# Performance work log

Measured on AMD Instinct MI355X. Metric: run time of the kernel, lower is better.

## Reference

```python
import jax, jax.numpy as jnp
import numpy as np

EPS = 1e-5
NEG_SLOPE = 0.01
GROUPS = 8


def leaky(x):
    return jnp.where(x >= 0, x, NEG_SLOPE * x)


def group_norm(x, gamma, beta):
    # torchsparse GroupNorm on a single-batch sparse tensor: normalize over
    # all points and the channels within each group. x: [N, C]
    N, C = x.shape
    xg = x.reshape(N, GROUPS, C // GROUPS)
    mean = xg.mean(axis=(0, 2), keepdims=True)
    var = xg.var(axis=(0, 2), keepdims=True)
    xn = ((xg - mean) * jax.lax.rsqrt(var + EPS)).reshape(N, C)
    return xn * gamma + beta


def spconv(feats, W, in_map, out_map, n_out):
    # Rulebook gather -> per-offset GEMM -> scatter-add.
    # feats: [N_in, Cin], W: [K, Cin, Cout], in_map/out_map: [K, M]
    Cout = W.shape[-1]
    g = feats[in_map]                               # [K, M, Cin] gather
    c = jnp.einsum('kmc,kcd->kmd', g, W)            # [K, M, Cout]
    out = jnp.zeros((n_out, Cout), feats.dtype)
    return out.at[out_map.reshape(-1)].add(c.reshape(-1, Cout))


def residual_block(h, Wa, ga, ba, Wb, gb, bb, m_in, m_out, n_out):
    y = group_norm(spconv(h, Wa, m_in, m_out, n_out), ga, ba)
    y = group_norm(spconv(y, Wb, m_in, m_out, n_out), gb, bb)
    return leaky(y + h)  # identity downsample (inc==outc, stride==1)


def setup_inputs() -> dict:
    key = jax.random.key(0)
    ks = jax.random.split(key, 12)
    N_in, N_out, C = 600000, 150000, 64
    M1, M2 = 75000, 60000
    sc = 0.05
    inp = {
        'x': jax.random.normal(ks[0], (N_in, C), jnp.float32),
        'W1': jax.random.normal(ks[1], (8, C, C), jnp.float32) * sc,
        'g1': jnp.ones((C,), jnp.float32), 'b1': jnp.zeros((C,), jnp.float32),
        'Wa1': jax.random.normal(ks[2], (27, C, C), jnp.float32) * sc,
        'ga1': jnp.ones((C,), jnp.float32), 'ba1': jnp.zeros((C,), jnp.float32),
        'Wb1': jax.random.normal(ks[3], (27, C, C), jnp.float32) * sc,
        'gb1': jnp.ones((C,), jnp.float32), 'bb1': jnp.zeros((C,), jnp.float32),
        'Wa2': jax.random.normal(ks[4], (27, C, C), jnp.float32) * sc,
        'ga2': jnp.ones((C,), jnp.float32), 'ba2': jnp.zeros((C,), jnp.float32),
        'Wb2': jax.random.normal(ks[5], (27, C, C), jnp.float32) * sc,
        'gb2': jnp.ones((C,), jnp.float32), 'bb2': jnp.zeros((C,), jnp.float32),
        'm1_in': jax.random.randint(ks[6], (8, M1), 0, N_in, jnp.int32),
        'm1_out': jax.random.randint(ks[7], (8, M1), 0, N_out, jnp.int32),
        'm2_in': jax.random.randint(ks[8], (27, M2), 0, N_out, jnp.int32),
        'm2_out': jax.random.randint(ks[9], (27, M2), 0, N_out, jnp.int32),
        'n_out': N_out,
    }
    return inp


def reference(x, W1, g1, b1, Wa1, ga1, ba1, Wb1, gb1, bb1,
              Wa2, ga2, ba2, Wb2, gb2, bb2,
              m1_in, m1_out, m2_in, m2_out, n_out):
    # BasicConvolutionBlock: Conv3d(ks=2, stride=2) -> GroupNorm(8) -> LeakyReLU
    h = leaky(group_norm(spconv(x, W1, m1_in, m1_out, n_out), g1, b1))
    # ResidualBlock x2: (Conv3d ks=3 -> GN -> Conv3d ks=3 -> GN) + identity, LeakyReLU
    h = residual_block(h, Wa1, ga1, ba1, Wb1, gb1, bb1, m2_in, m2_out, n_out)
    h = residual_block(h, Wa2, ga2, ba2, Wb2, gb2, bb2, m2_in, m2_out, n_out)
    return h
```

## Files before the change

### kernel.cpp

```cpp
#include <hip/hip_runtime.h>

#define NEG_SLOPE 0.01f
#define GN_EPS 1e-5f

typedef __attribute__((ext_vector_type(8))) __bf16 bf16x8;
typedef __attribute__((ext_vector_type(4))) __bf16 bf16x4;
typedef __attribute__((ext_vector_type(4))) float f32x4;
typedef __attribute__((ext_vector_type(2))) unsigned uintx2;

__device__ __forceinline__ float bf_lo(unsigned v) { return __uint_as_float(v << 16); }
__device__ __forceinline__ float bf_hi(unsigned v) { return __uint_as_float(v & 0xffff0000u); }

__global__ __launch_bounds__(256) void hist_kernel(
    const int* __restrict__ om, int* __restrict__ cnt, int E)
{
    const int stride = gridDim.x * blockDim.x;
    for (int e = blockIdx.x * blockDim.x + threadIdx.x; e < E; e += stride)
        atomicAdd(&cnt[om[e]], 1);
}

__global__ __launch_bounds__(256) void scan1_kernel(
    const int* __restrict__ cnt, int* __restrict__ part, int N)
{
    __shared__ int ls[256];
    int b = blockIdx.x, t = threadIdx.x;
    int i0 = b * 1024 + t * 4, s = 0;
#pragma unroll
    for (int u = 0; u < 4; ++u) if (i0 + u < N) s += cnt[i0 + u];
    ls[t] = s; __syncthreads();
    for (int off = 128; off > 0; off >>= 1) {
        if (t < off) ls[t] += ls[t + off];
        __syncthreads();
    }
    if (t == 0) part[b] = ls[0];
}

__global__ void scan2_kernel(int* __restrict__ part, int nb)
{
    if (blockIdx.x == 0 && threadIdx.x == 0) {
        int run = 0;
        for (int i = 0; i < nb; ++i) { int v = part[i]; part[i] = run; run += v; }
    }
}

__global__ __launch_bounds__(256) void scan3_kernel(
    const int* __restrict__ cnt, const int* __restrict__ part,
    int* __restrict__ base, int N)
{
    __shared__ int ls[256];
    int b = blockIdx.x, t = threadIdx.x;
    int i0 = b * 1024 + t * 4;
    int v0 = 0, v1 = 0, v2 = 0, v3 = 0;
    if (i0 + 0 < N) v0 = cnt[i0 + 0];
    if (i0 + 1 < N) v1 = cnt[i0 + 1];
    if (i0 + 2 < N) v2 = cnt[i0 + 2];
    if (i0 + 3 < N) v3 = cnt[i0 + 3];
    int s = v0 + v1 + v2 + v3;
    ls[t] = s; __syncthreads();
    for (int off = 1; off < 256; off <<= 1) {
        int x = (t >= off) ? ls[t - off] : 0;
        __syncthreads();
        ls[t] += x;
        __syncthreads();
    }
    int run = part[b] + ls[t] - s;
    if (i0 + 0 < N) { base[i0 + 0] = run; run += v0; if (i0 + 0 == N - 1) base[N] = run; }
    if (i0 + 1 < N) { base[i0 + 1] = run; run += v1; if (i0 + 1 == N - 1) base[N] = run; }
    if (i0 + 2 < N) { base[i0 + 2] = run; run += v2; if (i0 + 2 == N - 1) base[N] = run; }
    if (i0 + 3 < N) { base[i0 + 3] = run; run += v3; if (i0 + 3 == N - 1) base[N] = run; }
}

__global__ __launch_bounds__(256) void scatter_kernel(
    const int* __restrict__ om, const int* __restrict__ base,
    int* __restrict__ cur, int* __restrict__ inv, int E)
{
    const int stride = gridDim.x * blockDim.x;
    for (int e = blockIdx.x * blockDim.x + threadIdx.x; e < E; e += stride) {
        int o = om[e];
        int p = base[o] + atomicAdd(&cur[o], 1);
        inv[e] = p;
    }
}

template<int F32IN>
__global__ __launch_bounds__(256) void conv_mfma_kernel(
    const void* __restrict__ feats, const float* __restrict__ W,
    const int* __restrict__ in_map, const int* __restrict__ inv,
    __bf16* __restrict__ C, int M, int BPK)
{
    const int lane = threadIdx.x & 63;
    const int wv   = threadIdx.x >> 6;
    const int k    = blockIdx.x / BPK;
    const int blk  = blockIdx.x % BPK;
    const int l15  = lane & 15;
    const int lg   = lane >> 4;

    const float* Wk = W + (size_t)k * 4096;
    bf16x8 b[4][2];
#pragma unroll
    for (int nt = 0; nt < 4; ++nt)
#pragma unroll
        for (int h = 0; h < 2; ++h)
#pragma unroll
            for (int j = 0; j < 8; ++j)
                b[nt][h][j] = (__bf16)Wk[(h * 32 + lg * 8 + j) * 64 + nt * 16 + l15];

    const int* imk   = in_map + (size_t)k * M;
    const int ntiles = (M + 15) >> 4;
    const int wpk    = BPK * 4;

    for (int t = blk * 4 + wv; t < ntiles; t += wpk) {
        int m  = t * 16 + l15;
        int mc = m < M ? m : M - 1;
        int ii = imk[mc];
        bf16x8 a0, a1;
        if (F32IN) {
            const float4* rp = (const float4*)((const float*)feats + (size_t)ii * 64 + lg * 8);
            float4 u0 = rp[0], u1 = rp[1];
            float4 u2 = rp[8], u3 = rp[9];
            a0[0] = (__bf16)u0.x; a0[1] = (__bf16)u0.y; a0[2] = (__bf16)u0.z; a0[3] = (__bf16)u0.w;
            a0[4] = (__bf16)u1.x; a0[5] = (__bf16)u1.y; a0[6] = (__bf16)u1.z; a0[7] = (__bf16)u1.w;
            a1[0] = (__bf16)u2.x; a1[1] = (__bf16)u2.y; a1[2] = (__bf16)u2.z; a1[3] = (__bf16)u2.w;
            a1[4] = (__bf16)u3.x; a1[5] = (__bf16)u3.y; a1[6] = (__bf16)u3.z; a1[7] = (__bf16)u3.w;
        } else {
            const bf16x8* rp = (const bf16x8*)((const __bf16*)feats + (size_t)ii * 64 + lg * 8);
            a0 = rp[0];
            a1 = rp[4];
        }
        f32x4 c0 = {0.f,0.f,0.f,0.f}, c1 = c0, c2 = c0, c3 = c0;
        c0 = __builtin_amdgcn_mfma_f32_16x16x32_bf16(a0, b[0][0], c0, 0, 0, 0);
        c1 = __builtin_amdgcn_mfma_f32_16x16x32_bf16(a0, b[1][0], c1, 0, 0, 0);
        c2 = __builtin_amdgcn_mfma_f32_16x16x32_bf16(a0, b[2][0], c2, 0, 0, 0);
        c3 = __builtin_amdgcn_mfma_f32_16x16x32_bf16(a0, b[3][0], c3, 0, 0, 0);
        c0 = __builtin_amdgcn_mfma_f32_16x16x32_bf16(a1, b[0][1], c0, 0, 0, 0);
        c1 = __builtin_amdgcn_mfma_f32_16x16x32_bf16(a1, b[1][1], c1, 0, 0, 0);
        c2 = __builtin_amdgcn_mfma_f32_16x16x32_bf16(a1, b[2][1], c2, 0, 0, 0);
        c3 = __builtin_amdgcn_mfma_f32_16x16x32_bf16(a1, b[3][1], c3, 0, 0, 0);

        const int e_base = k * M + t * 16;
        f32x4 cc[4] = {c0, c1, c2, c3};
#pragma unroll
        for (int r = 0; r < 4; ++r) {
            int row = lg * 4 + r;
            if (t * 16 + row < M) {
                int p = inv[e_base + row];
                __bf16* cr = C + (size_t)p * 64 + l15;
#pragma unroll
                for (int nt = 0; nt < 4; ++nt) {
                    __bf16 v = (__bf16)cc[nt][r];
                    __builtin_nontemporal_store(v, cr + nt * 16);
                }
            }
        }
    }
}

__global__ __launch_bounds__(256) void reduce_kernel(
    const unsigned* __restrict__ C2, const int* __restrict__ base,
    float* __restrict__ out, float* __restrict__ stats, int N)
{
    const int lane = threadIdx.x & 63;
    const int wv   = threadIdx.x >> 6;
    const int rq   = lane >> 4;
    const int cq   = lane & 15;
    float rs = 0.f, rqsum = 0.f;

    const int ostride = gridDim.x * 4;
    for (int o = blockIdx.x * 4 + wv; o < N; o += ostride) {
        const int s = base[o], t = base[o + 1];
        float a0 = 0.f, a1 = 0.f, a2 = 0.f, a3 = 0.f;
        for (int i = s + rq; i < t; i += 4) {
            uintx2 v = __builtin_nontemporal_load(
                (const uintx2*)(C2 + (size_t)i * 32 + cq * 2));
            a0 += bf_lo(v.x); a1 += bf_hi(v.x);
            a2 += bf_lo(v.y); a3 += bf_hi(v.y);
        }
        a0 += __shfl_xor(a0, 16); a1 += __shfl_xor(a1, 16);
        a2 += __shfl_xor(a2, 16); a3 += __shfl_xor(a3, 16);
        a0 += __shfl_xor(a0, 32); a1 += __shfl_xor(a1, 32);
        a2 += __shfl_xor(a2, 32); a3 += __shfl_xor(a3, 32);
        if (rq == 0) {
            float4 r = {a0, a1, a2, a3};
            *(float4*)(out + (size_t)o * 64 + cq * 4) = r;
            rs    += (a0 + a1) + (a2 + a3);
            rqsum += (a0 * a0 + a1 * a1) + (a2 * a2 + a3 * a3);
        }
    }
    rs += __shfl_xor(rs, 1); rqsum += __shfl_xor(rqsum, 1);
    __shared__ float ls[4][16];
    if (rq == 0 && (cq & 1) == 0) {
        ls[wv][cq >> 1] = rs;
        ls[wv][8 + (cq >> 1)] = rqsum;
    }
    __syncthreads();
    if (threadIdx.x < 16) {
        float t = (ls[0][threadIdx.x] + ls[1][threadIdx.x]) +
                  (ls[2][threadIdx.x] + ls[3][threadIdx.x]);
        unsafeAtomicAdd(stats + threadIdx.x, t);
    }
}

__global__ __launch_bounds__(256) void conv_kernel(
    const float* __restrict__ feats, const float* __restrict__ W,
    const int* __restrict__ in_map, const int* __restrict__ out_map,
    float* __restrict__ out, int M, int BPK)
{
    const int lane = threadIdx.x & 63;
    const int wv   = threadIdx.x >> 6;
    const int k    = blockIdx.x / BPK;
    const int blk  = blockIdx.x % BPK;
    const float* Wk = W + (size_t)k * 4096;
    float w[64];
#pragma unroll
    for (int c = 0; c < 64; ++c) w[c] = Wk[c * 64 + lane];
    __shared__ float fbuf[4][64];
    const int* im = in_map + (size_t)k * M;
    const int* om = out_map + (size_t)k * M;
    const int stride = BPK * 4;
    for (int m = blk * 4 + wv; m < M; m += stride) {
        int ii = im[m];
        int oi = om[m];
        float f = feats[(size_t)ii * 64 + lane];
        fbuf[wv][lane] = f;
        const float* fb = fbuf[wv];
        float a0 = 0.f, a1 = 0.f, a2 = 0.f, a3 = 0.f;
#pragma unroll
        for (int c = 0; c < 64; c += 4) {
            float4 f4 = *(const float4*)(fb + c);
            a0 = fmaf(f4.x, w[c + 0], a0);
            a1 = fmaf(f4.y, w[c + 1], a1);
            a2 = fmaf(f4.z, w[c + 2], a2);
            a3 = fmaf(f4.w, w[c + 3], a3);
        }
        unsafeAtomicAdd(out + (size_t)oi * 64 + lane, (a0 + a1) + (a2 + a3));
    }
}

__global__ __launch_bounds__(256) void gn_stats_kernel(
    const float4* __restrict__ x, float* __restrict__ stats, long total4)
{
    const int lane = threadIdx.x & 63;
    float s = 0.f, q = 0.f;
    const long stride = (long)gridDim.x * blockDim.x;
    for (long i = (long)blockIdx.x * blockDim.x + threadIdx.x; i < total4; i += stride) {
        float4 v = x[i];
        s += (v.x + v.y) + (v.z + v.w);
        q += (v.x * v.x + v.y * v.y) + (v.z * v.z + v.w * v.w);
    }
    s += __shfl_xor(s, 1);  q += __shfl_xor(q, 1);
    s += __shfl_xor(s, 16); q += __shfl_xor(q, 16);
    s += __shfl_xor(s, 32); q += __shfl_xor(q, 32);
    __shared__ float ls[4][16];
    const int wv = threadIdx.x >> 6;
    const int g = (lane >> 1) & 7;
    if (lane < 16 && (lane & 1) == 0) { ls[wv][g] = s; ls[wv][8 + g] = q; }
    __syncthreads();
    if (threadIdx.x < 16) {
        float t = (ls[0][threadIdx.x] + ls[1][threadIdx.x]) +
                  (ls[2][threadIdx.x] + ls[3][threadIdx.x]);
        unsafeAtomicAdd(stats + threadIdx.x, t);
    }
}

__global__ __launch_bounds__(256) void gn_apply_kernel(
    const float4* __restrict__ x, const float* __restrict__ stats,
    const float* __restrict__ gamma, const float* __restrict__ beta,
    const float4* resid, float4* out_f, bf16x4* out_bf,
    long total4, float invc, int do_leaky)
{
    __shared__ float sc[64], sh[64];
    if (threadIdx.x < 64) {
        int c = threadIdx.x, g = c >> 3;
        float mean = stats[g] * invc;
        float var  = fmaf(-mean, mean, stats[8 + g] * invc);
        float s    = rsqrtf(var + GN_EPS) * gamma[c];
        sc[c] = s;
        sh[c] = fmaf(-mean, s, beta[c]);
    }
    __syncthreads();
    const long stride = (long)gridDim.x * blockDim.x;
    for (long i = (long)blockIdx.x * blockDim.x + threadIdx.x; i < total4; i += stride) {
        float4 v = x[i];
        int c0 = ((int)(i & 15)) << 2;
        float4 r;
        r.x = fmaf(v.x, sc[c0 + 0], sh[c0 + 0]);
        r.y = fmaf(v.y, sc[c0 + 1], sh[c0 + 1]);
        r.z = fmaf(v.z, sc[c0 + 2], sh[c0 + 2]);
        r.w = fmaf(v.w, sc[c0 + 3], sh[c0 + 3]);
        if (resid) {
            float4 h4 = resid[i];
            r.x += h4.x; r.y += h4.y; r.z += h4.z; r.w += h4.w;
        }
        if (do_leaky) {
            r.x = r.x >= 0.f ? r.x : NEG_SLOPE * r.x;
            r.y = r.y >= 0.f ? r.y : NEG_SLOPE * r.y;
            r.z = r.z >= 0.f ? r.z : NEG_SLOPE * r.z;
            r.w = r.w >= 0.f ? r.w : NEG_SLOPE * r.w;
        }
        if (out_f) out_f[i] = r;
        if (out_bf) {
            bf16x4 o;
            o.x = (__bf16)r.x; o.y = (__bf16)r.y; o.z = (__bf16)r.z; o.w = (__bf16)r.w;
            out_bf[i] = o;
        }
    }
}

extern "C" void kernel_launch(void* const* d_in, const int* in_sizes, int n_in,
                              void* d_out, int out_size, void* d_ws, size_t ws_size,
                              hipStream_t stream) {
    const float* x   = (const float*)d_in[0];
    const float* W1  = (const float*)d_in[1];
    const float* g1  = (const float*)d_in[2];
    const float* b1  = (const float*)d_in[3];
    const float* Wa1 = (const float*)d_in[4];
    const float* ga1 = (const float*)d_in[5];
    const float* ba1 = (const float*)d_in[6];
    const float* Wb1 = (const float*)d_in[7];
    const float* gb1 = (const float*)d_in[8];
    const float* bb1 = (const float*)d_in[9];
    const float* Wa2 = (const float*)d_in[10];
    const float* ga2 = (const float*)d_in[11];
    const float* ba2 = (const float*)d_in[12];
    const float* Wb2 = (const float*)d_in[13];
    const float* gb2 = (const float*)d_in[14];
    const float* bb2 = (const float*)d_in[15];
    const int* m1_in  = (const int*)d_in[16];
    const int* m1_out = (const int*)d_in[17];
    const int* m2_in  = (const int*)d_in[18];
    const int* m2_out = (const int*)d_in[19];

    const int N   = out_size / 64;
    const int M1  = in_sizes[16] / 8;
    const int M2  = in_sizes[18] / 27;
    const int E1  = 8 * M1;
    const int E2  = 27 * M2;
    const int Emax = E1 > E2 ? E1 : E2;

    float* h = (float*)d_out;
    const long  total4 = (long)N * 16;
    const float invc   = 1.f / ((float)N * 8.f);

    char* wp = (char*)d_ws;
    size_t off = 0;
    auto alloc = [&](size_t bytes) {
        void* p = wp + off;
        off = (off + bytes + 255) & ~(size_t)255;
        return p;
    };
    float*  acc   = (float*)alloc((size_t)N * 64 * 4);
    __bf16* hbf   = (__bf16*)alloc((size_t)N * 64 * 2);
    __bf16* ybf   = (__bf16*)alloc((size_t)N * 64 * 2);
    __bf16* Cbuf  = (__bf16*)alloc((size_t)Emax * 64 * 2);
    int*    base1 = (int*)alloc((size_t)(N + 1) * 4);
    int*    base2 = (int*)alloc((size_t)(N + 1) * 4);
    int*    cnt   = (int*)alloc((size_t)N * 4);
    int*    part  = (int*)alloc(4096);
    int*    inv1  = (int*)alloc((size_t)E1 * 4);
    int*    inv2  = (int*)alloc((size_t)E2 * 4);
    float*  stats = (float*)alloc(5 * 16 * 4);
    const size_t need = off;

    if (ws_size < need) {
        float* y  = (float*)Cbuf;
        float* st = stats;
        const size_t nbytes = (size_t)N * 64 * 4;
        auto convL = [&](const float* feats, const float* W, const int* im,
                         const int* om, int K, int M, int BPK) {
            hipMemsetAsync(acc, 0, nbytes, stream);
            conv_kernel<<<dim3(K * BPK), 256, 0, stream>>>(feats, W, im, om, acc, M, BPK);
        };
        auto gnL = [&](const float* gamma, const float* beta, const float* resid,
                       float* outp, int leaky) {
            hipMemsetAsync(st, 0, 16 * sizeof(float), stream);
            gn_stats_kernel<<<1024, 256, 0, stream>>>((const float4*)acc, st, total4);
            gn_apply_kernel<<<1024, 256, 0, stream>>>((const float4*)acc, st, gamma, beta,
                                                      (const float4*)resid, (float4*)outp,
                                                      nullptr, total4, invc, leaky);
        };
        convL(x, W1, m1_in, m1_out, 8, M1, 320); gnL(g1, b1, nullptr, h, 1);
        convL(h, Wa1, m2_in, m2_out, 27, M2, 96); gnL(ga1, ba1, nullptr, y, 0);
        convL(y, Wb1, m2_in, m2_out, 27, M2, 96); gnL(gb1, bb1, h, h, 1);
        convL(h, Wa2, m2_in, m2_out, 27, M2, 96); gnL(ga2, ba2, nullptr, y, 0);
        convL(y, Wb2, m2_in, m2_out, 27, M2, 96); gnL(gb2, bb2, h, h, 1);
        return;
    }

    hipMemsetAsync(stats, 0, 5 * 16 * sizeof(float), stream);

    const int nb = (N + 1023) / 1024;
    auto buildCSR = [&](const int* om, int E, int* base, int* inv) {
        hipMemsetAsync(cnt, 0, (size_t)N * 4, stream);
        hist_kernel<<<2048, 256, 0, stream>>>(om, cnt, E);
        scan1_kernel<<<nb, 256, 0, stream>>>(cnt, part, N);
        scan2_kernel<<<1, 64, 0, stream>>>(part, nb);
        scan3_kernel<<<nb, 256, 0, stream>>>(cnt, part, base, N);
        hipMemsetAsync(cnt, 0, (size_t)N * 4, stream);
        scatter_kernel<<<2048, 256, 0, stream>>>(om, base, cnt, inv, E);
    };
    buildCSR(m1_out, E1, base1, inv1);
    buildCSR(m2_out, E2, base2, inv2);

    float* st0  = stats;
    float* stA1 = stats + 16;
    float* stB1 = stats + 32;
    float* stA2 = stats + 48;
    float* stB2 = stats + 64;

    auto conv = [&](const void* feats, int f32in, const float* W, const int* im,
                    int K, int M, int BPK, const int* base, const int* inv,
                    float* statOut) {
        dim3 grid(K * BPK);
        if (f32in)
            conv_mfma_kernel<1><<<grid, 256, 0, stream>>>(feats, W, im, inv, Cbuf, M, BPK);
        else
            conv_mfma_kernel<0><<<grid, 256, 0, stream>>>(feats, W, im, inv, Cbuf, M, BPK);
        reduce_kernel<<<2048, 256, 0, stream>>>((const unsigned*)Cbuf, base,
                                                acc, statOut, N);
    };
    auto gn = [&](const float* st, const float* gamma, const float* beta,
                  const float* resid, float* outf, __bf16* outbf, int leaky) {
        gn_apply_kernel<<<1024, 256, 0, stream>>>((const float4*)acc, st, gamma, beta,
                                                  (const float4*)resid, (float4*)outf,
                                                  (bf16x4*)outbf, total4, invc, leaky);
    };

    conv(x, 1, W1, m1_in, 8, M1, 256, base1, inv1, st0);
    gn(st0, g1, b1, nullptr, h, hbf, 1);
    conv(hbf, 0, Wa1, m2_in, 27, M2, 96, base2, inv2, stA1);
    gn(stA1, ga1, ba1, nullptr, nullptr, ybf, 0);
    conv(ybf, 0, Wb1, m2_in, 27, M2, 96, base2, inv2, stB1);
    gn(stB1, gb1, bb1, h, h, hbf, 1);
    conv(hbf, 0, Wa2, m2_in, 27, M2, 96, base2, inv2, stA2);
    gn(stA2, ga2, ba2, nullptr, nullptr, ybf, 0);
    conv(ybf, 0, Wb2, m2_in, 27, M2, 96, base2, inv2, stB2);
    gn(stB2, gb2, bb2, h, h, nullptr, 1);
}
```

Baseline: 1.078 ms.

## Bin rulebook entries by output tile and offset to localize conv scatter writes

Adds a second counting-sort pass that groups rulebook entries by (output-row tile of 1024, kernel offset). The MFMA conv kernel then runs one block per bin, so each block's scattered writes into the CSR-ordered C buffer fall in a narrow address range, which should improve write locality. The reduce output accumulator also moves from fp32 to bf16, roughly halving that traffic at some precision cost in the pre-GroupNorm values. The price is extra preprocessing kernels and index arrays, plus load imbalance from many small bins.

After: 1.635 ms. 1.52x slower.

```diff
diff --git a/kernel.cpp b/kernel.cpp
--- a/kernel.cpp
+++ b/kernel.cpp
@@ -2,6 +2,7 @@
 
 #define NEG_SLOPE 0.01f
 #define GN_EPS 1e-5f
+#define SSH 10
 
 typedef __attribute__((ext_vector_type(8))) __bf16 bf16x8;
 typedef __attribute__((ext_vector_type(4))) __bf16 bf16x4;
@@ -82,18 +83,47 @@
     }
 }
 
+__global__ __launch_bounds__(256) void histB_kernel(
+    const int* __restrict__ om, int* __restrict__ cnt, int M, int TK, int BPK)
+{
+    int k = blockIdx.x / BPK, blk = blockIdx.x % BPK;
+    const int* omk = om + (size_t)k * M;
+    for (int m = blk * 256 + threadIdx.x; m < M; m += BPK * 256)
+        atomicAdd(&cnt[(omk[m] >> SSH) * TK + k], 1);
+}
+
+__global__ __launch_bounds__(256) void scatterB_kernel(
+    const int* __restrict__ om, const int* __restrict__ im,
+    const int* __restrict__ inv, const int* __restrict__ baseB,
+    int* __restrict__ curB, int* __restrict__ im2, int* __restrict__ pv2,
+    int M, int TK, int BPK)
+{
+    int k = blockIdx.x / BPK, blk = blockIdx.x % BPK;
+    const int* omk  = om  + (size_t)k * M;
+    const int* imk  = im  + (size_t)k * M;
+    const int* invk = inv + (size_t)k * M;
+    for (int m = blk * 256 + threadIdx.x; m < M; m += BPK * 256) {
+        int key = (omk[m] >> SSH) * TK + k;
+        int pos = baseB[key] + atomicAdd(&curB[key], 1);
+        im2[pos] = imk[m];
+        pv2[pos] = invk[m];
+    }
+}
+
 template<int F32IN>
-__global__ __launch_bounds__(256) void conv_mfma_kernel(
+__global__ __launch_bounds__(256) void conv_bin_kernel(
     const void* __restrict__ feats, const float* __restrict__ W,
-    const int* __restrict__ in_map, const int* __restrict__ inv,
-    __bf16* __restrict__ C, int M, int BPK)
-{
+    const int* __restrict__ im2, const int* __restrict__ pv2,
+    const int* __restrict__ baseB, __bf16* __restrict__ C, int TK)
+{
+    const int bin  = blockIdx.x;
+    const int k    = bin % TK;
     const int lane = threadIdx.x & 63;
     const int wv   = threadIdx.x >> 6;
-    const int k    = blockIdx.x / BPK;
-    const int blk  = blockIdx.x % BPK;
     const int l15  = lane & 15;
     const int lg   = lane >> 4;
+    const int s = baseB[bin], e = baseB[bin + 1];
+    if (s >= e) return;
 
     const float* Wk = W + (size_t)k * 4096;
     bf16x8 b[4][2];
@@ -105,14 +135,11 @@
             for (int j = 0; j < 8; ++j)
                 b[nt][h][j] = (__bf16)Wk[(h * 32 + lg * 8 + j) * 64 + nt * 16 + l15];
 
-    const int* imk   = in_map + (size_t)k * M;
-    const int ntiles = (M + 15) >> 4;
-    const int wpk    = BPK * 4;
-
-    for (int t = blk * 4 + wv; t < ntiles; t += wpk) {
-        int m  = t * 16 + l15;
-        int mc = m < M ? m : M - 1;
-        int ii = imk[mc];
+    for (int cb = s + wv * 16; cb < e; cb += 64) {
+        const int idx = cb + l15;
+        const int idc = idx < e ? idx : e - 1;
+        const int ii  = im2[idc];
+        const int pv  = pv2[idc];
         bf16x8 a0, a1;
         if (F32IN) {
             const float4* rp = (const float4*)((const float*)feats + (size_t)ii * 64 + lg * 8);
@@ -137,13 +164,12 @@
         c2 = __builtin_amdgcn_mfma_f32_16x16x32_bf16(a1, b[2][1], c2, 0, 0, 0);
         c3 = __builtin_amdgcn_mfma_f32_16x16x32_bf16(a1, b[3][1], c3, 0, 0, 0);
 
-        const int e_base = k * M + t * 16;
         f32x4 cc[4] = {c0, c1, c2, c3};
 #pragma unroll
         for (int r = 0; r < 4; ++r) {
-            int row = lg * 4 + r;
-            if (t * 16 + row < M) {
-                int p = inv[e_base + row];
+            const int row = lg * 4 + r;
+            if (cb + row < e) {
+                int p = __shfl(pv, row);
                 __bf16* cr = C + (size_t)p * 64 + l15;
 #pragma unroll
                 for (int nt = 0; nt < 4; ++nt) {
@@ -157,7 +183,7 @@
 
 __global__ __launch_bounds__(256) void reduce_kernel(
     const unsigned* __restrict__ C2, const int* __restrict__ base,
-    float* __restrict__ out, float* __restrict__ stats, int N)
+    __bf16* __restrict__ out, float* __restrict__ stats, int N)
 {
     const int lane = threadIdx.x & 63;
     const int wv   = threadIdx.x >> 6;
@@ -180,8 +206,9 @@
         a0 += __shfl_xor(a0, 32); a1 += __shfl_xor(a1, 32);
         a2 += __shfl_xor(a2, 32); a3 += __shfl_xor(a3, 32);
         if (rq == 0) {
-            float4 r = {a0, a1, a2, a3};
-            *(float4*)(out + (size_t)o * 64 + cq * 4) = r;
+            bf16x4 r;
+            r.x = (__bf16)a0; r.y = (__bf16)a1; r.z = (__bf16)a2; r.w = (__bf16)a3;
+            *(bf16x4*)(out + (size_t)o * 64 + cq * 4) = r;
             rs    += (a0 + a1) + (a2 + a3);
             rqsum += (a0 * a0 + a1 * a1) + (a2 * a2 + a3 * a3);
         }
@@ -197,6 +224,57 @@
         float t = (ls[0][threadIdx.x] + ls[1][threadIdx.x]) +
                   (ls[2][threadIdx.x] + ls[3][threadIdx.x]);
         unsafeAtomicAdd(stats + threadIdx.x, t);
+    }
+}
+
+template<int BFIN>
+__global__ __launch_bounds__(256) void gn_apply_kernel(
+    const void* __restrict__ xin, const float* __restrict__ stats,
+    const float* __restrict__ gamma, const float* __restrict__ beta,
+    const float4* resid, float4* out_f, bf16x4* out_bf,
+    long total4, float invc, int do_leaky)
+{
+    __shared__ float sc[64], sh[64];
+    if (threadIdx.x < 64) {
+        int c = threadIdx.x, g = c >> 3;
+        float mean = stats[g] * invc;
+        float var  = fmaf(-mean, mean, stats[8 + g] * invc);
+        float s    = rsqrtf(var + GN_EPS) * gamma[c];
+        sc[c] = s;
+        sh[c] = fmaf(-mean, s, beta[c]);
+    }
+    __syncthreads();
+    const long stride = (long)gridDim.x * blockDim.x;
+    for (long i = (long)blockIdx.x * blockDim.x + threadIdx.x; i < total4; i += stride) {
+        float4 v;
+        if (BFIN) {
+            bf16x4 u = ((const bf16x4*)xin)[i];
+            v.x = (float)u.x; v.y = (float)u.y; v.z = (float)u.z; v.w = (float)u.w;
+        } else {
+            v = ((const float4*)xin)[i];
+        }
+        int c0 = ((int)(i & 15)) << 2;
+        float4 r;
+        r.x = fmaf(v.x, sc[c0 + 0], sh[c0 + 0]);
+        r.y = fmaf(v.y, sc[c0 + 1], sh[c0 + 1]);
+        r.z = fmaf(v.z, sc[c0 + 2], sh[c0 + 2]);
+        r.w = fmaf(v.w, sc[c0 + 3], sh[c0 + 3]);
+        if (resid) {
+            float4 h4 = resid[i];
+            r.x += h4.x; r.y += h4.y; r.z += h4.z; r.w += h4.w;
+        }
+        if (do_leaky) {
+            r.x = r.x >= 0.f ? r.x : NEG_SLOPE * r.x;
+            r.y = r.y >= 0.f ? r.y : NEG_SLOPE * r.y;
+            r.z = r.z >= 0.f ? r.z : NEG_SLOPE * r.z;
+            r.w = r.w >= 0.f ? r.w : NEG_SLOPE * r.w;
+        }
+        if (out_f) out_f[i] = r;
+        if (out_bf) {
+            bf16x4 o;
+            o.x = (__bf16)r.x; o.y = (__bf16)r.y; o.z = (__bf16)r.z; o.w = (__bf16)r.w;
+            out_bf[i] = o;
+        }
     }
 }
 
@@ -259,50 +337,6 @@
         float t = (ls[0][threadIdx.x] + ls[1][threadIdx.x]) +
                   (ls[2][threadIdx.x] + ls[3][threadIdx.x]);
         unsafeAtomicAdd(stats + threadIdx.x, t);
-    }
-}
-
-__global__ __launch_bounds__(256) void gn_apply_kernel(
-    const float4* __restrict__ x, const float* __restrict__ stats,
-    const float* __restrict__ gamma, const float* __restrict__ beta,
-    const float4* resid, float4* out_f, bf16x4* out_bf,
-    long total4, float invc, int do_leaky)
-{
-    __shared__ float sc[64], sh[64];
-    if (threadIdx.x < 64) {
-        int c = threadIdx.x, g = c >> 3;
-        float mean = stats[g] * invc;
-        float var  = fmaf(-mean, mean, stats[8 + g] * invc);
-        float s    = rsqrtf(var + GN_EPS) * gamma[c];
-        sc[c] = s;
-        sh[c] = fmaf(-mean, s, beta[c]);
-    }
-    __syncthreads();
-    const long stride = (long)gridDim.x * blockDim.x;
-    for (long i = (long)blockIdx.x * blockDim.x + threadIdx.x; i < total4; i += stride) {
-        float4 v = x[i];
-        int c0 = ((int)(i & 15)) << 2;
-        float4 r;
-        r.x = fmaf(v.x, sc[c0 + 0], sh[c0 + 0]);
-        r.y = fmaf(v.y, sc[c0 + 1], sh[c0 + 1]);
-        r.z = fmaf(v.z, sc[c0 + 2], sh[c0 + 2]);
-        r.w = fmaf(v.w, sc[c0 + 3], sh[c0 + 3]);
-        if (resid) {
-            float4 h4 = resid[i];
-            r.x += h4.x; r.y += h4.y; r.z += h4.z; r.w += h4.w;
-        }
-        if (do_leaky) {
-            r.x = r.x >= 0.f ? r.x : NEG_SLOPE * r.x;
-            r.y = r.y >= 0.f ? r.y : NEG_SLOPE * r.y;
-            r.z = r.z >= 0.f ? r.z : NEG_SLOPE * r.z;
-            r.w = r.w >= 0.f ? r.w : NEG_SLOPE * r.w;
-        }
-        if (out_f) out_f[i] = r;
-        if (out_bf) {
-            bf16x4 o;
-            o.x = (__bf16)r.x; o.y = (__bf16)r.y; o.z = (__bf16)r.z; o.w = (__bf16)r.w;
-            out_bf[i] = o;
-        }
     }
 }
 
@@ -336,6 +370,9 @@
     const int E1  = 8 * M1;
     const int E2  = 27 * M2;
     const int Emax = E1 > E2 ? E1 : E2;
+    const int tilesS = (N + (1 << SSH) - 1) >> SSH;
+    const int NB1 = tilesS * 8;
+    const int NB2 = tilesS * 27;
 
     float* h = (float*)d_out;
     const long  total4 = (long)N * 16;
@@ -348,58 +385,80 @@
         off = (off + bytes + 255) & ~(size_t)255;
         return p;
     };
-    float*  acc   = (float*)alloc((size_t)N * 64 * 4);
-    __bf16* hbf   = (__bf16*)alloc((size_t)N * 64 * 2);
-    __bf16* ybf   = (__bf16*)alloc((size_t)N * 64 * 2);
-    __bf16* Cbuf  = (__bf16*)alloc((size_t)Emax * 64 * 2);
-    int*    base1 = (int*)alloc((size_t)(N + 1) * 4);
-    int*    base2 = (int*)alloc((size_t)(N + 1) * 4);
-    int*    cnt   = (int*)alloc((size_t)N * 4);
-    int*    part  = (int*)alloc(4096);
-    int*    inv1  = (int*)alloc((size_t)E1 * 4);
-    int*    inv2  = (int*)alloc((size_t)E2 * 4);
-    float*  stats = (float*)alloc(5 * 16 * 4);
+    __bf16* accbf  = (__bf16*)alloc((size_t)N * 64 * 2);
+    __bf16* hbf    = (__bf16*)alloc((size_t)N * 64 * 2);
+    __bf16* ybf    = (__bf16*)alloc((size_t)N * 64 * 2);
+    __bf16* Cbuf   = (__bf16*)alloc((size_t)Emax * 64 * 2);
+    int*    base1  = (int*)alloc((size_t)(N + 1) * 4);
+    int*    base2  = (int*)alloc((size_t)(N + 1) * 4);
+    int*    cnt    = (int*)alloc((size_t)N * 4);
+    int*    part   = (int*)alloc(4096);
+    int*    inv1   = (int*)alloc((size_t)E1 * 4);
+    int*    inv2   = (int*)alloc((size_t)E2 * 4);
+    int*    baseB1 = (int*)alloc((size_t)(NB1 + 1) * 4);
+    int*    baseB2 = (int*)alloc((size_t)(NB2 + 1) * 4);
+    int*    im2_1  = (int*)alloc((size_t)E1 * 4);
+    int*    pv2_1  = (int*)alloc((size_t)E1 * 4);
+    int*    im2_2  = (int*)alloc((size_t)E2 * 4);
+    int*    pv2_2  = (int*)alloc((size_t)E2 * 4);
+    float*  stats  = (float*)alloc(5 * 16 * 4);
     const size_t need = off;
 
     if (ws_size < need) {
-        float* y  = (float*)Cbuf;
-        float* st = stats;
+        float* accF = (float*)d_ws;
+        float* yF   = accF + (size_t)N * 64;
+        float* stF  = yF + (size_t)N * 64;
         const size_t nbytes = (size_t)N * 64 * 4;
         auto convL = [&](const float* feats, const float* W, const int* im,
                          const int* om, int K, int M, int BPK) {
-            hipMemsetAsync(acc, 0, nbytes, stream);
-            conv_kernel<<<dim3(K * BPK), 256, 0, stream>>>(feats, W, im, om, acc, M, BPK);
+            hipMemsetAsync(accF, 0, nbytes, stream);
+            conv_kernel<<<dim3(K * BPK), 256, 0, stream>>>(feats, W, im, om, accF, M, BPK);
         };
         auto gnL = [&](const float* gamma, const float* beta, const float* resid,
                        float* outp, int leaky) {
-            hipMemsetAsync(st, 0, 16 * sizeof(float), stream);
-            gn_stats_kernel<<<1024, 256, 0, stream>>>((const float4*)acc, st, total4);
-            gn_apply_kernel<<<1024, 256, 0, stream>>>((const float4*)acc, st, gamma, beta,
-                                                      (const float4*)resid, (float4*)outp,
-                                                      nullptr, total4, invc, leaky);
+            hipMemsetAsync(stF, 0, 16 * sizeof(float), stream);
+            gn_stats_kernel<<<1024, 256, 0, stream>>>((const float4*)accF, stF, total4);
+            gn_apply_kernel<0><<<1024, 256, 0, stream>>>(accF, stF, gamma, beta,
+                                                         (const float4*)resid, (float4*)outp,
+                                                         nullptr, total4, invc, leaky);
         };
         convL(x, W1, m1_in, m1_out, 8, M1, 320); gnL(g1, b1, nullptr, h, 1);
-        convL(h, Wa1, m2_in, m2_out, 27, M2, 96); gnL(ga1, ba1, nullptr, y, 0);
-        convL(y, Wb1, m2_in, m2_out, 27, M2, 96); gnL(gb1, bb1, h, h, 1);
-        convL(h, Wa2, m2_in, m2_out, 27, M2, 96); gnL(ga2, ba2, nullptr, y, 0);
-        convL(y, Wb2, m2_in, m2_out, 27, M2, 96); gnL(gb2, bb2, h, h, 1);
+        convL(h, Wa1, m2_in, m2_out, 27, M2, 96); gnL(ga1, ba1, nullptr, yF, 0);
+        convL(yF, Wb1, m2_in, m2_out, 27, M2, 96); gnL(gb1, bb1, h, h, 1);
+        convL(h, Wa2, m2_in, m2_out, 27, M2, 96); gnL(ga2, ba2, nullptr, yF, 0);
+        convL(yF, Wb2, m2_in, m2_out, 27, M2, 96); gnL(gb2, bb2, h, h, 1);
         return;
     }
 
     hipMemsetAsync(stats, 0, 5 * 16 * sizeof(float), stream);
 
-    const int nb = (N + 1023) / 1024;
+    const int nbN = (N + 1023) / 1024;
     auto buildCSR = [&](const int* om, int E, int* base, int* inv) {
         hipMemsetAsync(cnt, 0, (size_t)N * 4, stream);
         hist_kernel<<<2048, 256, 0, stream>>>(om, cnt, E);
-        scan1_kernel<<<nb, 256, 0, stream>>>(cnt, part, N);
-        scan2_kernel<<<1, 64, 0, stream>>>(part, nb);
-        scan3_kernel<<<nb, 256, 0, stream>>>(cnt, part, base, N);
+        scan1_kernel<<<nbN, 256, 0, stream>>>(cnt, part, N);
+        scan2_kernel<<<1, 64, 0, stream>>>(part, nbN);
+        scan3_kernel<<<nbN, 256, 0, stream>>>(cnt, part, base, N);
         hipMemsetAsync(cnt, 0, (size_t)N * 4, stream);
         scatter_kernel<<<2048, 256, 0, stream>>>(om, base, cnt, inv, E);
     };
+    auto buildBins = [&](const int* om, const int* im, const int* inv, int M,
+                         int TK, int NB, int* baseB, int* im2, int* pv2) {
+        const int BPK = 48;
+        const int nbB = (NB + 1023) / 1024;
+        hipMemsetAsync(cnt, 0, (size_t)NB * 4, stream);
+        histB_kernel<<<dim3(TK * BPK), 256, 0, stream>>>(om, cnt, M, TK, BPK);
+        scan1_kernel<<<nbB, 256, 0, stream>>>(cnt, part, NB);
+        scan2_kernel<<<1, 64, 0, stream>>>(part, nbB);
+        scan3_kernel<<<nbB, 256, 0, stream>>>(cnt, part, baseB, NB);
+        hipMemsetAsync(cnt, 0, (size_t)NB * 4, stream);
+        scatterB_kernel<<<dim3(TK * BPK), 256, 0, stream>>>(om, im, inv, baseB, cnt,
+                                                            im2, pv2, M, TK, BPK);
+    };
     buildCSR(m1_out, E1, base1, inv1);
     buildCSR(m2_out, E2, base2, inv2);
+    buildBins(m1_out, m1_in, inv1, M1, 8, NB1, baseB1, im2_1, pv2_1);
+    buildBins(m2_out, m2_in, inv2, M2, 27, NB2, baseB2, im2_2, pv2_2);
 
     float* st0  = stats;
     float* stA1 = stats + 16;
@@ -407,32 +466,31 @@
     float* stA2 = stats + 48;
     float* stB2 = stats + 64;
 
-    auto conv = [&](const void* feats, int f32in, const float* W, const int* im,
-                    int K, int M, int BPK, const int* base, const int* inv,
-                    float* statOut) {
-        dim3 grid(K * BPK);
+    auto conv = [&](const void* feats, int f32in, const float* W, int TK, int NB,
+                    const int* im2, const int* pv2, const int* baseB,
+                    const int* base, float* statOut) {
         if (f32in)
-            conv_mfma_kernel<1><<<grid, 256, 0, stream>>>(feats, W, im, inv, Cbuf, M, BPK);
+            conv_bin_kernel<1><<<NB, 256, 0, stream>>>(feats, W, im2, pv2, baseB, Cbuf, TK);
         else
-            conv_mfma_kernel<0><<<grid, 256, 0, stream>>>(feats, W, im, inv, Cbuf, M, BPK);
+            conv_bin_kernel<0><<<NB, 256, 0, stream>>>(feats, W, im2, pv2, baseB, Cbuf, TK);
         reduce_kernel<<<2048, 256, 0, stream>>>((const unsigned*)Cbuf, base,
-                                                acc, statOut, N);
+                                                accbf, statOut, N);
     };
     auto gn = [&](const float* st, const float* gamma, const float* beta,
                   const float* resid, float* outf, __bf16* outbf, int leaky) {
-        gn_apply_kernel<<<1024, 256, 0, stream>>>((const float4*)acc, st, gamma, beta,
-                                                  (const float4*)resid, (float4*)outf,
-                                                  (bf16x4*)outbf, total4, invc, leaky);
+        gn_apply_kernel<1><<<1024, 256, 0, stream>>>(accbf, st, gamma, beta,
+                                                     (const float4*)resid, (float4*)outf,
+                                                     (bf16x4*)outbf, total4, invc, leaky);
     };
 
-    conv(x, 1, W1, m1_in, 8, M1, 256, base1, inv1, st0);
+    conv(x, 1, W1, 8, NB1, im2_1, pv2_1, baseB1, base1, st0);
     gn(st0, g1, b1, nullptr, h, hbf, 1);
-    conv(hbf, 0, Wa1, m2_in, 27, M2, 96, base2, inv2, stA1);
+    conv(hbf, 0, Wa1, 27, NB2, im2_2, pv2_2, baseB2, base2, stA1);
     gn(stA1, ga1, ba1, nullptr, nullptr, ybf, 0);
-    conv(ybf, 0, Wb1, m2_in, 27, M2, 96, base2, inv2, stB1);
+    conv(ybf, 0, Wb1, 27, NB2, im2_2, pv2_2, baseB2, base2, stB1);
     gn(stB1, gb1, bb1, h, h, hbf, 1);
-    conv(hbf, 0, Wa2, m2_in, 27, M2, 96, base2, inv2, stA2);
+    conv(hbf, 0, Wa2, 27, NB2, im2_2, pv2_2, baseB2, base2, stA2);
     gn(stA2, ga2, ba2, nullptr, nullptr, ybf, 0);
-    conv(ybf, 0, Wb2, m2_in, 27, M2, 96, base2, inv2, stB2);
+    conv(ybf, 0, Wb2, 27, NB2, im2_2, pv2_2, baseB2, base2, stB2);
     gn(stB2, gb2, bb2, h, h, nullptr, 1);
 }
```
